# Kernel tuning notes

Hardware: AMD Instinct MI355X
Metric: run time of the kernel (lower is better)

Reference implementation:

```python
import jax, jax.numpy as jnp
import numpy as np

N_IMG = 1024
N_VIEWS = 90


def _bilinear(img, yi, xi):
    """Bilinear sample img at float coords (yi=row, xi=col); 0 outside (skimage warp cval=0)."""
    n = img.shape[0]
    y0 = jnp.floor(yi)
    x0 = jnp.floor(xi)
    wy = yi - y0
    wx = xi - x0
    y0i = y0.astype(jnp.int32)
    x0i = x0.astype(jnp.int32)

    def get(yy, xx):
        valid = (yy >= 0) & (yy < n) & (xx >= 0) & (xx < n)
        v = img[jnp.clip(yy, 0, n - 1), jnp.clip(xx, 0, n - 1)]
        return jnp.where(valid, v, jnp.zeros((), img.dtype))

    v00 = get(y0i, x0i)
    v01 = get(y0i, x0i + 1)
    v10 = get(y0i + 1, x0i)
    v11 = get(y0i + 1, x0i + 1)
    return (v00 * (1 - wy) * (1 - wx) + v01 * (1 - wy) * wx
            + v10 * wy * (1 - wx) + v11 * wy * wx)


def radon_jax(image, theta_deg):
    """skimage.transform.radon(image, theta, circle=True) equivalent.
    Rotate image by each angle (bilinear, about center = N//2, inverse map as in
    skimage warp) and sum over rows. Returns sinogram [N, n_angles]."""
    n = image.shape[0]
    center = n // 2
    ang = jnp.deg2rad(theta_deg.astype(image.dtype))
    cos_a = jnp.cos(ang)  # [A]
    sin_a = jnp.sin(ang)
    coords = jnp.arange(n, dtype=image.dtype)
    X, Y = jnp.meshgrid(coords, coords)  # X = col (x), Y = row (y), [N, N]

    def rotate_and_sum(ca, sa):
        # inverse map: src = R @ dst (homogeneous, (x, y) order) as in skimage radon
        x_in = ca * X + sa * Y - center * (ca + sa - 1)
        y_in = -sa * X + ca * Y - center * (ca - sa - 1)
        rotated = _bilinear(image, y_in, x_in)  # [N, N]
        return rotated.sum(axis=0)  # sum over rows -> projection [N]

    sino = jax.vmap(rotate_and_sum)(cos_a, sin_a)  # [A, N]
    return sino.T  # [N, A] to match skimage radon layout


def setup_inputs() -> dict:
    key = jax.random.key(0)
    k1, _ = jax.random.split(key)
    x = jax.random.normal(k1, (N_IMG, N_IMG), dtype=jnp.float32)
    theta = jnp.arange(N_VIEWS, dtype=jnp.float32) * 2.0  # 0..178 deg, 2-deg spacing
    return {"x": x, "theta": theta}


def reference(x, theta):
    return radon_jax(x, theta)
```

## Files before the change

kernel.cpp:

```cpp
#include <hip/hip_runtime.h>

#define N_IMG   1024
#define N_VIEWS 90
#define CENTER  512
#define TILE    64
#define NYB     (N_IMG / TILE)
#define MAXH    92

__device__ __forceinline__ void map_coords(float ca, float sa, float cx, float cy,
                                           float Xf, float Yf,
                                           float& x_in, float& y_in) {
    const float fx0 = fmaf(ca, Xf, cx);
    const float fy0 = fmaf(-sa, Xf, cy);
    x_in = fmaf(sa, Yf, fx0);
    y_in = fmaf(ca, Yf, fy0);
}

__device__ __forceinline__ void gload_lds4(const float* g, float* l) {
    __builtin_amdgcn_global_load_lds((const __attribute__((address_space(1))) void*)g,
                                     (__attribute__((address_space(3))) void*)l,
                                     4, 0, 0);
}

template<int STRIDE>
__global__ __launch_bounds__(256) void radon_tile(const float* __restrict__ img,
                                                  const float* __restrict__ theta,
                                                  float* __restrict__ partial,
                                                  float* __restrict__ out,
                                                  int a0, int mode) {
    __shared__ float tile[MAXH * STRIDE];
    __shared__ float red[4][64];

    const int a  = a0 + blockIdx.z;
    const int X0 = blockIdx.x * TILE;
    const int Y0 = blockIdx.y * TILE;
    const int tid  = threadIdx.x;
    const int lane = tid & 63;
    const int wv   = tid >> 6;

    float* __restrict__ pslot = partial + ((size_t)(a * NYB + blockIdx.y) << 10) + X0;

    const float ang = theta[a] * 0.017453292519943295f;
    float sa, ca;
    __sincosf(ang, &sa, &ca);
    const float cx = (float)CENTER * (1.0f - ca - sa);
    const float cy = (float)CENTER * (1.0f - ca + sa);

    float x00, y00, x01, y01, x10, y10, x11, y11;
    map_coords(ca, sa, cx, cy, (float)X0,        (float)Y0,        x00, y00);
    map_coords(ca, sa, cx, cy, (float)(X0 + 63), (float)Y0,        x01, y01);
    map_coords(ca, sa, cx, cy, (float)X0,        (float)(Y0 + 63), x10, y10);
    map_coords(ca, sa, cx, cy, (float)(X0 + 63), (float)(Y0 + 63), x11, y11);
    const float xmin = fminf(fminf(x00, x01), fminf(x10, x11));
    const float xmax = fmaxf(fmaxf(x00, x01), fmaxf(x10, x11));
    const float ymin = fminf(fminf(y00, y01), fminf(y10, y11));
    const float ymax = fmaxf(fmaxf(y00, y01), fmaxf(y10, y11));

    const int ix0_raw = (int)floorf(xmin);
    const int ix1_raw = (int)floorf(xmax) + 1;
    const int iy0_raw = (int)floorf(ymin);
    const int iy1_raw = (int)floorf(ymax) + 1;

    const int ix0 = max(0, ix0_raw);
    const int ix1 = min(N_IMG - 1, ix1_raw);
    const int iy0 = max(0, iy0_raw);
    const int iy1 = min(N_IMG - 1, iy1_raw);

    if (ix1 < ix0 || iy1 < iy0) {
        if (mode == 0) { if (tid < 64) pslot[tid] = 0.0f; }
        return;
    }

    const int a0x = min(ix0, N_IMG - 64);
    const int b0x = max(a0x, ix1 - 63);
    const int dB  = b0x - a0x;
    const int h   = iy1 - iy0 + 1;

    {
        const float* g = img + (size_t)(iy0 + wv) * N_IMG + a0x + lane;
        float* l = tile + wv * STRIDE;
        for (int r = wv; r < h; r += 4) {
            gload_lds4(g, l);
            if (dB > 0) gload_lds4(g + dB, l + dB);
            g += 4 * N_IMG;
            l += 4 * STRIDE;
        }
    }
    __syncthreads();

    const int X = X0 + lane;
    const float Xf  = (float)X;
    const float fx0 = fmaf(ca, Xf, cx);
    const float fy0 = fmaf(-sa, Xf, cy);
    const int Ybase = Y0 + wv * 16;
    float acc = 0.0f;

    const bool interior = (ix0_raw >= 0) && (ix1_raw <= N_IMG - 1) &&
                          (iy0_raw >= 0) && (iy1_raw <= N_IMG - 1);
    const int base = -(iy0 * STRIDE + a0x);

    if (interior) {
        #pragma unroll
        for (int i = 0; i < 16; ++i) {
            const float Yf   = (float)(Ybase + i);
            const float x_in = fmaf(sa, Yf, fx0);
            const float y_in = fmaf(ca, Yf, fy0);
            const float x0f = floorf(x_in);
            const float y0f = floorf(y_in);
            const float wx  = x_in - x0f;
            const float wy  = y_in - y0f;
            const int li = (int)y0f * STRIDE + (int)x0f + base;
            const float t00 = tile[li];
            const float t01 = tile[li + 1];
            const float t10 = tile[li + STRIDE];
            const float t11 = tile[li + STRIDE + 1];
            const float top = fmaf(wx, t01 - t00, t00);
            const float bot = fmaf(wx, t11 - t10, t10);
            acc += fmaf(wy, bot - top, top);
        }
    } else {
        #pragma unroll
        for (int i = 0; i < 16; ++i) {
            const float Yf   = (float)(Ybase + i);
            const float x_in = fmaf(sa, Yf, fx0);
            const float y_in = fmaf(ca, Yf, fy0);
            const float x0f = floorf(x_in);
            const float y0f = floorf(y_in);
            const float wx  = x_in - x0f;
            const float wy  = y_in - y0f;
            const int x0 = (int)x0f;
            const int y0 = (int)y0f;
            const int x0c = min(max(x0,     0), N_IMG - 1);
            const int x1c = min(max(x0 + 1, 0), N_IMG - 1);
            const int y0c = min(max(y0,     0), N_IMG - 1);
            const int y1c = min(max(y0 + 1, 0), N_IMG - 1);
            const float wxa = (x0     >= 0 && x0     < N_IMG) ? (1.0f - wx) : 0.0f;
            const float wxb = (x0 + 1 >= 0 && x0 + 1 < N_IMG) ? wx          : 0.0f;
            const float wya = (y0     >= 0 && y0     < N_IMG) ? (1.0f - wy) : 0.0f;
            const float wyb = (y0 + 1 >= 0 && y0 + 1 < N_IMG) ? wy          : 0.0f;
            const int r0 = (y0c - iy0) * STRIDE - a0x;
            const int r1 = (y1c - iy0) * STRIDE - a0x;
            const float t00 = tile[r0 + x0c];
            const float t01 = tile[r0 + x1c];
            const float t10 = tile[r1 + x0c];
            const float t11 = tile[r1 + x1c];
            acc += wya * fmaf(wxa, t00, wxb * t01)
                 + wyb * fmaf(wxa, t10, wxb * t11);
        }
    }

    red[wv][lane] = acc;
    __syncthreads();
    if (wv == 0) {
        const float s = red[0][lane] + red[1][lane] + red[2][lane] + red[3][lane];
        if (mode == 0) pslot[lane] = s;
        else           atomicAdd(&out[X * N_VIEWS + a], s);
    }
}

__global__ __launch_bounds__(256) void reduce_partials(const float* __restrict__ partial,
                                                       float* __restrict__ out) {
    const int g = blockIdx.x * 256 + threadIdx.x;
    const int a = g >> 10;
    const int X = g & 1023;
    float s = 0.0f;
    #pragma unroll
    for (int yb = 0; yb < NYB; ++yb)
        s += partial[((size_t)(a * NYB + yb) << 10) + X];
    out[X * N_VIEWS + a] = s;
}

extern "C" void kernel_launch(void* const* d_in, const int* in_sizes, int n_in,
                              void* d_out, int out_size, void* d_ws, size_t ws_size,
                              hipStream_t stream) {
    const float* img   = (const float*)d_in[0];
    const float* theta = (const float*)d_in[1];
    float* out     = (float*)d_out;
    float* partial = (float*)d_ws;

    const size_t needed = (size_t)N_VIEWS * NYB * N_IMG * sizeof(float);
    const int mode = (ws_size >= needed) ? 0 : 1;
    if (mode == 1)
        hipMemsetAsync(d_out, 0, (size_t)out_size * sizeof(float), stream);

    dim3 grid(N_IMG / TILE, N_IMG / TILE, N_VIEWS / 2);
    radon_tile<95><<<grid, 256, 0, stream>>>(img, theta, partial, out, 0, mode);
    radon_tile<97><<<grid, 256, 0, stream>>>(img, theta, partial, out, 45, mode);

    if (mode == 0)
        reduce_partials<<<(N_VIEWS * N_IMG) / 256, 256, 0, stream>>>(partial, out);
}
```

Baseline: 159.0 us.

## Merge angle-split launches into one 512-thread kernel with runtime stride select

The two per-half-angle launches become a single launch over all 90 angles. Each block now has 8 waves, each doing 8 rows instead of 16, and the LDS stride (95 or 97) is chosen at runtime from the sign of cos. The cross-wave reduction reuses the tile LDS buffer instead of a separate array. This removes a launch boundary and the tail between launches and gives more parallelism per block, at the cost of fewer rows per thread to hide LDS latency, more sync overhead, and possible occupancy changes from the larger blocks.

```diff
diff --git a/kernel.cpp b/kernel.cpp
--- a/kernel.cpp
+++ b/kernel.cpp
@@ -6,6 +6,9 @@
 #define TILE    64
 #define NYB     (N_IMG / TILE)
 #define MAXH    92
+#define MAXS    97
+#define NTHREADS 512
+#define NWAVES   8
 
 __device__ __forceinline__ void map_coords(float ca, float sa, float cx, float cy,
                                            float Xf, float Yf,
@@ -23,85 +26,30 @@
 }
 
 template<int STRIDE>
-__global__ __launch_bounds__(256) void radon_tile(const float* __restrict__ img,
-                                                  const float* __restrict__ theta,
-                                                  float* __restrict__ partial,
-                                                  float* __restrict__ out,
-                                                  int a0, int mode) {
-    __shared__ float tile[MAXH * STRIDE];
-    __shared__ float red[4][64];
-
-    const int a  = a0 + blockIdx.z;
-    const int X0 = blockIdx.x * TILE;
-    const int Y0 = blockIdx.y * TILE;
-    const int tid  = threadIdx.x;
-    const int lane = tid & 63;
-    const int wv   = tid >> 6;
-
-    float* __restrict__ pslot = partial + ((size_t)(a * NYB + blockIdx.y) << 10) + X0;
-
-    const float ang = theta[a] * 0.017453292519943295f;
-    float sa, ca;
-    __sincosf(ang, &sa, &ca);
-    const float cx = (float)CENTER * (1.0f - ca - sa);
-    const float cy = (float)CENTER * (1.0f - ca + sa);
-
-    float x00, y00, x01, y01, x10, y10, x11, y11;
-    map_coords(ca, sa, cx, cy, (float)X0,        (float)Y0,        x00, y00);
-    map_coords(ca, sa, cx, cy, (float)(X0 + 63), (float)Y0,        x01, y01);
-    map_coords(ca, sa, cx, cy, (float)X0,        (float)(Y0 + 63), x10, y10);
-    map_coords(ca, sa, cx, cy, (float)(X0 + 63), (float)(Y0 + 63), x11, y11);
-    const float xmin = fminf(fminf(x00, x01), fminf(x10, x11));
-    const float xmax = fmaxf(fmaxf(x00, x01), fmaxf(x10, x11));
-    const float ymin = fminf(fminf(y00, y01), fminf(y10, y11));
-    const float ymax = fmaxf(fmaxf(y00, y01), fmaxf(y10, y11));
-
-    const int ix0_raw = (int)floorf(xmin);
-    const int ix1_raw = (int)floorf(xmax) + 1;
-    const int iy0_raw = (int)floorf(ymin);
-    const int iy1_raw = (int)floorf(ymax) + 1;
-
-    const int ix0 = max(0, ix0_raw);
-    const int ix1 = min(N_IMG - 1, ix1_raw);
-    const int iy0 = max(0, iy0_raw);
-    const int iy1 = min(N_IMG - 1, iy1_raw);
-
-    if (ix1 < ix0 || iy1 < iy0) {
-        if (mode == 0) { if (tid < 64) pslot[tid] = 0.0f; }
-        return;
-    }
-
-    const int a0x = min(ix0, N_IMG - 64);
-    const int b0x = max(a0x, ix1 - 63);
-    const int dB  = b0x - a0x;
-    const int h   = iy1 - iy0 + 1;
-
+__device__ __forceinline__ float tile_work(const float* __restrict__ img,
+                                           float* __restrict__ tile,
+                                           int lane, int wv,
+                                           int iy0, int h, int a0x, int dB,
+                                           float sa, float ca, float fx0, float fy0,
+                                           int Ybase, bool interior) {
     {
         const float* g = img + (size_t)(iy0 + wv) * N_IMG + a0x + lane;
         float* l = tile + wv * STRIDE;
-        for (int r = wv; r < h; r += 4) {
+        for (int r = wv; r < h; r += NWAVES) {
             gload_lds4(g, l);
             if (dB > 0) gload_lds4(g + dB, l + dB);
-            g += 4 * N_IMG;
-            l += 4 * STRIDE;
+            g += NWAVES * N_IMG;
+            l += NWAVES * STRIDE;
         }
     }
     __syncthreads();
 
-    const int X = X0 + lane;
-    const float Xf  = (float)X;
-    const float fx0 = fmaf(ca, Xf, cx);
-    const float fy0 = fmaf(-sa, Xf, cy);
-    const int Ybase = Y0 + wv * 16;
     float acc = 0.0f;
-
-    const bool interior = (ix0_raw >= 0) && (ix1_raw <= N_IMG - 1) &&
-                          (iy0_raw >= 0) && (iy1_raw <= N_IMG - 1);
     const int base = -(iy0 * STRIDE + a0x);
 
     if (interior) {
         #pragma unroll
-        for (int i = 0; i < 16; ++i) {
+        for (int i = 0; i < TILE / NWAVES; ++i) {
             const float Yf   = (float)(Ybase + i);
             const float x_in = fmaf(sa, Yf, fx0);
             const float y_in = fmaf(ca, Yf, fy0);
@@ -120,7 +68,7 @@
         }
     } else {
         #pragma unroll
-        for (int i = 0; i < 16; ++i) {
+        for (int i = 0; i < TILE / NWAVES; ++i) {
             const float Yf   = (float)(Ybase + i);
             const float x_in = fmaf(sa, Yf, fx0);
             const float y_in = fmaf(ca, Yf, fy0);
@@ -148,11 +96,85 @@
                  + wyb * fmaf(wxa, t10, wxb * t11);
         }
     }
-
-    red[wv][lane] = acc;
+    return acc;
+}
+
+__global__ __launch_bounds__(NTHREADS) void radon_tile(const float* __restrict__ img,
+                                                       const float* __restrict__ theta,
+                                                       float* __restrict__ partial,
+                                                       float* __restrict__ out,
+                                                       int mode) {
+    __shared__ float tile[MAXH * MAXS];
+
+    const int a  = blockIdx.z;
+    const int X0 = blockIdx.x * TILE;
+    const int Y0 = blockIdx.y * TILE;
+    const int tid  = threadIdx.x;
+    const int lane = tid & 63;
+    const int wv   = tid >> 6;
+
+    float* __restrict__ pslot = partial + ((size_t)(a * NYB + blockIdx.y) << 10) + X0;
+
+    const float ang = theta[a] * 0.017453292519943295f;
+    float sa, ca;
+    __sincosf(ang, &sa, &ca);
+    const float cx = (float)CENTER * (1.0f - ca - sa);
+    const float cy = (float)CENTER * (1.0f - ca + sa);
+
+    float x00, y00, x01, y01, x10, y10, x11, y11;
+    map_coords(ca, sa, cx, cy, (float)X0,        (float)Y0,        x00, y00);
+    map_coords(ca, sa, cx, cy, (float)(X0 + 63), (float)Y0,        x01, y01);
+    map_coords(ca, sa, cx, cy, (float)X0,        (float)(Y0 + 63), x10, y10);
+    map_coords(ca, sa, cx, cy, (float)(X0 + 63), (float)(Y0 + 63), x11, y11);
+    const float xmin = fminf(fminf(x00, x01), fminf(x10, x11));
+    const float xmax = fmaxf(fmaxf(x00, x01), fmaxf(x10, x11));
+    const float ymin = fminf(fminf(y00, y01), fminf(y10, y11));
+    const float ymax = fmaxf(fmaxf(y00, y01), fmaxf(y10, y11));
+
+    const int ix0_raw = (int)floorf(xmin);
+    const int ix1_raw = (int)floorf(xmax) + 1;
+    const int iy0_raw = (int)floorf(ymin);
+    const int iy1_raw = (int)floorf(ymax) + 1;
+
+    const int ix0 = max(0, ix0_raw);
+    const int ix1 = min(N_IMG - 1, ix1_raw);
+    const int iy0 = max(0, iy0_raw);
+    const int iy1 = min(N_IMG - 1, iy1_raw);
+
+    if (ix1 < ix0 || iy1 < iy0) {
+        if (mode == 0) { if (tid < 64) pslot[tid] = 0.0f; }
+        return;
+    }
+
+    const int a0x = min(ix0, N_IMG - 64);
+    const int b0x = max(a0x, ix1 - 63);
+    const int dB  = b0x - a0x;
+    const int h   = iy1 - iy0 + 1;
+
+    const int X = X0 + lane;
+    const float Xf  = (float)X;
+    const float fx0 = fmaf(ca, Xf, cx);
+    const float fy0 = fmaf(-sa, Xf, cy);
+    const int Ybase = Y0 + wv * (TILE / NWAVES);
+
+    const bool interior = (ix0_raw >= 0) && (ix1_raw <= N_IMG - 1) &&
+                          (iy0_raw >= 0) && (iy1_raw <= N_IMG - 1);
+
+    float acc;
+    if (ca > 0.0f)
+        acc = tile_work<95>(img, tile, lane, wv, iy0, h, a0x, dB,
+                            sa, ca, fx0, fy0, Ybase, interior);
+    else
+        acc = tile_work<97>(img, tile, lane, wv, iy0, h, a0x, dB,
+                            sa, ca, fx0, fy0, Ybase, interior);
+
+    __syncthreads();
+    tile[wv * 64 + lane] = acc;
     __syncthreads();
     if (wv == 0) {
-        const float s = red[0][lane] + red[1][lane] + red[2][lane] + red[3][lane];
+        float s = 0.0f;
+        #pragma unroll
+        for (int w = 0; w < NWAVES; ++w) s += tile[w * 64 + lane];
         if (mode == 0) pslot[lane] = s;
         else           atomicAdd(&out[X * N_VIEWS + a], s);
     }
@@ -183,9 +205,8 @@
     if (mode == 1)
         hipMemsetAsync(d_out, 0, (size_t)out_size * sizeof(float), stream);
 
-    dim3 grid(N_IMG / TILE, N_IMG / TILE, N_VIEWS / 2);
-    radon_tile<95><<<grid, 256, 0, stream>>>(img, theta, partial, out, 0, mode);
-    radon_tile<97><<<grid, 256, 0, stream>>>(img, theta, partial, out, 45, mode);
+    dim3 grid(N_IMG / TILE, N_IMG / TILE, N_VIEWS);
+    radon_tile<<<grid, NTHREADS, 0, stream>>>(img, theta, partial, out, mode);
 
     if (mode == 0)
         reduce_partials<<<(N_VIEWS * N_IMG) / 256, 256, 0, stream>>>(partial, out);
```

New measurement: 150.7 us. 5.3% less time.
